# Kernel optimization log

Hardware: AMD Instinct MI355X
Metric: run time of the kernel (lower is better)

## Reference

```python
import jax, jax.numpy as jnp
import numpy as np

EPS = 1e-7


def ciou_pairwise(b1, b2):
    # b1: (N,1,4), b2: (1,N,4) in xyxy; returns (N,N) CIoU
    b1x1, b1y1, b1x2, b1y2 = b1[..., 0], b1[..., 1], b1[..., 2], b1[..., 3]
    b2x1, b2y1, b2x2, b2y2 = b2[..., 0], b2[..., 1], b2[..., 2], b2[..., 3]

    # intersection
    iw = jnp.clip(jnp.minimum(b1x2, b2x2) - jnp.maximum(b1x1, b2x1), 0.0)
    ih = jnp.clip(jnp.minimum(b1y2, b2y2) - jnp.maximum(b1y1, b2y1), 0.0)
    inter = iw * ih

    w1, h1 = b1x2 - b1x1, b1y2 - b1y1
    w2, h2 = b2x2 - b2x1, b2y2 - b2y1
    union = w1 * h1 + w2 * h2 - inter + EPS
    iou = inter / union

    # smallest enclosing box diagonal
    cw = jnp.maximum(b1x2, b2x2) - jnp.minimum(b1x1, b2x1)
    ch = jnp.maximum(b1y2, b2y2) - jnp.minimum(b1y1, b2y1)
    c2 = cw * cw + ch * ch + EPS

    # squared center distance
    rho2 = ((b2x1 + b2x2 - b1x1 - b1x2) ** 2 + (b2y1 + b2y2 - b1y1 - b1y2) ** 2) / 4.0

    # aspect-ratio consistency term
    v = (4.0 / (np.pi ** 2)) * (jnp.arctan(w2 / (h2 + EPS)) - jnp.arctan(w1 / (h1 + EPS))) ** 2
    alpha = jax.lax.stop_gradient(v / (v - iou + (1.0 + EPS)))
    return iou - (rho2 / c2 + v * alpha)


def setup_inputs() -> dict:
    key = jax.random.key(0)
    k1, k2, k3 = jax.random.split(key, 3)
    N = 4096
    conf = jax.random.uniform(k1, (N, 1), dtype=jnp.float32)           # confidence in [0,1)
    xy1 = jax.random.uniform(k2, (N, 2), dtype=jnp.float32) * 600.0    # top-left corner
    wh = jax.random.uniform(k3, (N, 2), dtype=jnp.float32) * 100.0 + 1.0  # width/height >= 1
    x = jnp.concatenate([conf, xy1, xy1 + wh], axis=1)                 # (N, 5): conf, x1, y1, x2, y2
    gamma = jnp.zeros((1,), dtype=jnp.float32)
    return {"x": x, "gamma": gamma}


def reference(x, gamma):
    boxes = x[:, 1:]
    conf = x[:, 0]
    iou = ciou_pairwise(boxes[:, None, :], boxes[None, :, :])          # (N, N)
    conf_matrix = conf[:, None] * conf[None, :]                        # (N, N) outer product
    attention = jax.nn.softmax(iou * conf_matrix, axis=-1)             # (N, N)
    x_prime = x * gamma + attention @ x                                # (N, 5)
    return jax.nn.sigmoid(x_prime)
```

## Files before the change

### kernel.cpp

```cpp
#include <hip/hip_runtime.h>
#include <math.h>

#define N 4096
#define FEPS 1e-7f
#define HEPS 5e-8f
#define BLK 256
#define JT 64
#define CH (N / JT)
#define N6 (N * 6)
#define KATAN 0.6366197723675814f
#define SQL2E 1.2011224087864498f


__global__ __launch_bounds__(BLK) void ciou_attn_kernel(
        const float* __restrict__ x,
        float* __restrict__ part) {
    __shared__ float4 jrec[CH * 3];
    const int tid = threadIdx.x;
    const int gb = blockIdx.x / JT;
    const int jt = blockIdx.x % JT;
    const int i = gb * BLK + tid;

    if (tid < CH) {
        int j = jt * CH + tid;
        float cf = x[j * 5 + 0], jx1 = x[j * 5 + 1], jy1 = x[j * 5 + 2];
        float jx2 = x[j * 5 + 3], jy2 = x[j * 5 + 4];
        float w = jx2 - jx1, h = jy2 - jy1;
        jrec[tid * 3 + 0] = make_float4(jx1, jy1, jx2, jy2);
        jrec[tid * 3 + 1] = make_float4((jx1 + jx2) * 0.5f, (jy1 + jy2) * 0.5f, w, h);
        jrec[tid * 3 + 2] = make_float4(fmaf(w, h, HEPS),
                                        KATAN * atanf(w / (h + FEPS)),
                                        cf * SQL2E, cf);
    }

    {
    }
    float cfr = x[i * 5 + 0];
    const float rx1 = x[i * 5 + 1], ry1 = x[i * 5 + 2];
    const float rx2 = x[i * 5 + 3], ry2 = x[i * 5 + 4];
    const float rw = rx2 - rx1, rh = ry2 - ry1;
    const float rhx = (rx1 + rx2) * 0.5f, rhy = (ry1 + ry2) * 0.5f;
    const float rareps = fmaf(rw, rh, HEPS);
    const float rat = KATAN * atanf(rw / (rh + FEPS));
    const float rcf2 = cfr * SQL2E;

    __syncthreads();

    float sum = 0.f, a0 = 0.f, a1 = 0.f, a2 = 0.f, a3 = 0.f, a4 = 0.f;
    const float ONEP = 1.f + FEPS;

    float4 A = jrec[0], B = jrec[1], C = jrec[2];
#pragma unroll 4
    for (int jj = 0; jj < CH; jj++) {
        const int nx = ((jj + 1) & (CH - 1)) * 3;
        float4 nA = jrec[nx + 0];
        float4 nB = jrec[nx + 1];
        float4 nC = jrec[nx + 2];

        float iwr = fminf(rx2, A.z) - fmaxf(rx1, A.x);
        float ihr = fminf(ry2, A.w) - fmaxf(ry1, A.y);
        float iw = fmaxf(iwr, 0.f);
        float ih = fmaxf(ihr, 0.f);
        float inter = iw * ih;
        float uni = (rareps + C.x) - inter;
        float cw = (rw + B.z) - iwr;
        float chh = (rh + B.w) - ihr;
        float c2 = fmaf(cw, cw, fmaf(chh, chh, FEPS));
        float dx = B.x - rhx;
        float dy = B.y - rhy;
        float rho2 = fmaf(dx, dx, dy * dy);
        float da = C.y - rat;
        float v = da * da;
        float P = fmaf(v + ONEP, uni, -inter);
        P = fmaxf(P, 1e-12f);
        float uc = uni * c2;
        float rr = __builtin_amdgcn_rcpf(uc * P);
        float t1 = fmaf(inter, c2, -(rho2 * uni));
        float vu = v * uni;
        float n2 = (vu * vu) * c2;
        float num = fmaf(t1, P, -n2);
        float s = (num * rr) * (rcf2 * C.z);
        float e = __builtin_amdgcn_exp2f(s);
        sum += e;
        a0 = fmaf(e, C.w, a0);
        a1 = fmaf(e, A.x, a1);
        a2 = fmaf(e, A.y, a2);
        a3 = fmaf(e, A.z, a3);
        a4 = fmaf(e, A.w, a4);

        A = nA; B = nB; C = nC;
    }

    float* p = part + (size_t)jt * N6 + (size_t)i * 6;
    p[0] = sum; p[1] = a0; p[2] = a1; p[3] = a2; p[4] = a3; p[5] = a4;
}

__global__ void epilogue_kernel(const float* __restrict__ x,
                                const float* __restrict__ gamma,
                                const float* __restrict__ part,
                                float* __restrict__ out) {
    int idx = blockIdx.x * blockDim.x + threadIdx.x;
    if (idx >= N * 5) return;
    int i = idx / 5, c = idx % 5;
    float se = 0.f, a = 0.f;
    const float* p = part + (size_t)i * 6;
#pragma unroll 8
    for (int jt = 0; jt < JT; jt++) {
        se += p[jt * (size_t)N6 + 0];
        a  += p[jt * (size_t)N6 + 1 + c];
    }
    float xp = x[idx] * gamma[0] + a / se;
    out[idx] = 1.f / (1.f + expf(-xp));
}

extern "C" void kernel_launch(void* const* d_in, const int* in_sizes, int n_in,
                              void* d_out, int out_size, void* d_ws, size_t ws_size,
                              hipStream_t stream) {
    const float* x = (const float*)d_in[0];
    const float* gamma = (const float*)d_in[1];
    float* out = (float*)d_out;
    float* part = (float*)d_ws;

    ciou_attn_kernel<<<(N / BLK) * JT, BLK, 0, stream>>>(x, part);
    epilogue_kernel<<<(N * 5 + 255) / 256, 256, 0, stream>>>(x, gamma, part, out);
}
```

Before: 83.70 us.

## Exploit pairwise symmetry with wave-level tile rotation via ds_bpermute

Computes each unordered box pair once by assigning waves to 64x64 tile pairs. Column boxes and column accumulators rotate across lanes with ds_bpermute, so both row and column softmax partials come from one exponent. This roughly halves the pairwise CIoU/exp work. In exchange it adds twelve cross-lane permutes per step, doubles the accumulation FMAs and the partial-sum workspace, and the epilogue now reduces over twice as many slots in a transposed, coalesced layout.

Result: slower. 95.06 us (+13.6%).

```diff
diff --git a/kernel.cpp b/kernel.cpp
--- a/kernel.cpp
+++ b/kernel.cpp
@@ -2,97 +2,119 @@
 #include <math.h>
 
 #define N 4096
+#define T 64
+#define NT (N / T)
+#define NSLOT (NT * 2)
 #define FEPS 1e-7f
 #define HEPS 5e-8f
 #define BLK 256
-#define JT 64
-#define CH (N / JT)
-#define N6 (N * 6)
 #define KATAN 0.6366197723675814f
 #define SQL2E 1.2011224087864498f
+#define ISQL2E 0.8325546111576977f
 
 
-__global__ __launch_bounds__(BLK) void ciou_attn_kernel(
+__device__ __forceinline__ float bperm(int addr, float v) {
+    return __int_as_float(__builtin_amdgcn_ds_bpermute(addr, __float_as_int(v)));
+}
+
+__global__ __launch_bounds__(BLK) void ciou_sym_kernel(
         const float* __restrict__ x,
         float* __restrict__ part) {
-    __shared__ float4 jrec[CH * 3];
-    const int tid = threadIdx.x;
-    const int gb = blockIdx.x / JT;
-    const int jt = blockIdx.x % JT;
-    const int i = gb * BLK + tid;
+    const int lane = threadIdx.x & 63;
+    const int w = blockIdx.x * (BLK / 64) + (threadIdx.x >> 6);
 
-    if (tid < CH) {
-        int j = jt * CH + tid;
-        float cf = x[j * 5 + 0], jx1 = x[j * 5 + 1], jy1 = x[j * 5 + 2];
-        float jx2 = x[j * 5 + 3], jy2 = x[j * 5 + 4];
-        float w = jx2 - jx1, h = jy2 - jy1;
-        jrec[tid * 3 + 0] = make_float4(jx1, jy1, jx2, jy2);
-        jrec[tid * 3 + 1] = make_float4((jx1 + jx2) * 0.5f, (jy1 + jy2) * 0.5f, w, h);
-        jrec[tid * 3 + 2] = make_float4(fmaf(w, h, HEPS),
-                                        KATAN * atanf(w / (h + FEPS)),
-                                        cf * SQL2E, cf);
+    int ta, tb, k0, iters, diag;
+    if (w < NT) {
+        ta = w; tb = w; k0 = 0; iters = T; diag = 1;
+    } else {
+        int m = w - NT;
+        int p = m >> 1, kh = m & 1;
+        int a = 0, rem = p;
+        while (rem >= NT - 1 - a) { rem -= NT - 1 - a; a++; }
+        ta = a; tb = a + 1 + rem; k0 = kh << 5; iters = 32; diag = 0;
     }
+    const int kh = k0 >> 5;
+    const int slot_row = diag ? (ta * 2)     : (tb * 2 + kh);
+    const int slot_col = diag ? (ta * 2 + 1) : (ta * 2 + kh);
 
-    {
-    }
-    float cfr = x[i * 5 + 0];
+    const int i = ta * T + lane;
+    const float rcf = x[i * 5 + 0];
     const float rx1 = x[i * 5 + 1], ry1 = x[i * 5 + 2];
     const float rx2 = x[i * 5 + 3], ry2 = x[i * 5 + 4];
     const float rw = rx2 - rx1, rh = ry2 - ry1;
     const float rhx = (rx1 + rx2) * 0.5f, rhy = (ry1 + ry2) * 0.5f;
     const float rareps = fmaf(rw, rh, HEPS);
     const float rat = KATAN * atanf(rw / (rh + FEPS));
-    const float rcf2 = cfr * SQL2E;
+    const float rcf2 = rcf * SQL2E;
 
-    __syncthreads();
+    const int j = tb * T + ((lane + k0) & 63);
+    float jx1 = x[j * 5 + 1], jy1 = x[j * 5 + 2];
+    float jx2 = x[j * 5 + 3], jy2 = x[j * 5 + 4];
+    float jat = KATAN * atanf((jx2 - jx1) / ((jy2 - jy1) + FEPS));
+    float jcf2 = x[j * 5 + 0] * SQL2E;
 
-    float sum = 0.f, a0 = 0.f, a1 = 0.f, a2 = 0.f, a3 = 0.f, a4 = 0.f;
+    const int nxt = ((lane + 1) & 63) * 4;
     const float ONEP = 1.f + FEPS;
 
-    float4 A = jrec[0], B = jrec[1], C = jrec[2];
-#pragma unroll 4
-    for (int jj = 0; jj < CH; jj++) {
-        const int nx = ((jj + 1) & (CH - 1)) * 3;
-        float4 nA = jrec[nx + 0];
-        float4 nB = jrec[nx + 1];
-        float4 nC = jrec[nx + 2];
+    float rs = 0.f, r0 = 0.f, r1 = 0.f, r2 = 0.f, r3 = 0.f, r4 = 0.f;
+    float cs = 0.f, c0 = 0.f, c1 = 0.f, c2a = 0.f, c3 = 0.f, c4 = 0.f;
 
-        float iwr = fminf(rx2, A.z) - fmaxf(rx1, A.x);
-        float ihr = fminf(ry2, A.w) - fmaxf(ry1, A.y);
-        float iw = fmaxf(iwr, 0.f);
-        float ih = fmaxf(ihr, 0.f);
-        float inter = iw * ih;
-        float uni = (rareps + C.x) - inter;
-        float cw = (rw + B.z) - iwr;
-        float chh = (rh + B.w) - ihr;
+#pragma unroll 2
+    for (int k = 0; k < iters; k++) {
+        float jw = jx2 - jx1, jh = jy2 - jy1;
+        float jareps = fmaf(jw, jh, HEPS);
+        float dx = fmaf(0.5f, jx1 + jx2, -rhx);
+        float dy = fmaf(0.5f, jy1 + jy2, -rhy);
+
+        float iwr = fminf(rx2, jx2) - fmaxf(rx1, jx1);
+        float ihr = fminf(ry2, jy2) - fmaxf(ry1, jy1);
+        float inter = fmaxf(iwr, 0.f) * fmaxf(ihr, 0.f);
+        float uni = (rareps + jareps) - inter;
+        float cw = (rw + jw) - iwr;
+        float chh = (rh + jh) - ihr;
         float c2 = fmaf(cw, cw, fmaf(chh, chh, FEPS));
-        float dx = B.x - rhx;
-        float dy = B.y - rhy;
         float rho2 = fmaf(dx, dx, dy * dy);
-        float da = C.y - rat;
+        float da = jat - rat;
         float v = da * da;
         float P = fmaf(v + ONEP, uni, -inter);
         P = fmaxf(P, 1e-12f);
-        float uc = uni * c2;
-        float rr = __builtin_amdgcn_rcpf(uc * P);
+        float rr = __builtin_amdgcn_rcpf(uni * c2 * P);
         float t1 = fmaf(inter, c2, -(rho2 * uni));
         float vu = v * uni;
-        float n2 = (vu * vu) * c2;
-        float num = fmaf(t1, P, -n2);
-        float s = (num * rr) * (rcf2 * C.z);
-        float e = __builtin_amdgcn_exp2f(s);
-        sum += e;
-        a0 = fmaf(e, C.w, a0);
-        a1 = fmaf(e, A.x, a1);
-        a2 = fmaf(e, A.y, a2);
-        a3 = fmaf(e, A.z, a3);
-        a4 = fmaf(e, A.w, a4);
+        float num = fmaf(t1, P, -((vu * vu) * c2));
+        float e = __builtin_amdgcn_exp2f((num * rr) * (rcf2 * jcf2));
 
-        A = nA; B = nB; C = nC;
+        rs += e;
+        r0 = fmaf(e, jcf2, r0);
+        r1 = fmaf(e, jx1, r1);
+        r2 = fmaf(e, jy1, r2);
+        r3 = fmaf(e, jx2, r3);
+        r4 = fmaf(e, jy2, r4);
+
+        cs += e;
+        c0 = fmaf(e, rcf, c0);
+        c1 = fmaf(e, rx1, c1);
+        c2a = fmaf(e, ry1, c2a);
+        c3 = fmaf(e, rx2, c3);
+        c4 = fmaf(e, ry2, c4);
+
+        jx1 = bperm(nxt, jx1); jy1 = bperm(nxt, jy1);
+        jx2 = bperm(nxt, jx2); jy2 = bperm(nxt, jy2);
+        jat = bperm(nxt, jat); jcf2 = bperm(nxt, jcf2);
+        cs = bperm(nxt, cs);   c0 = bperm(nxt, c0);  c1 = bperm(nxt, c1);
+        c2a = bperm(nxt, c2a); c3 = bperm(nxt, c3);  c4 = bperm(nxt, c4);
     }
 
-    float* p = part + (size_t)jt * N6 + (size_t)i * 6;
-    p[0] = sum; p[1] = a0; p[2] = a1; p[3] = a2; p[4] = a3; p[5] = a4;
+    r0 *= ISQL2E;
+    float* pr = part + (size_t)slot_row * 6 * N;
+    pr[0 * N + i] = rs; pr[1 * N + i] = r0; pr[2 * N + i] = r1;
+    pr[3 * N + i] = r2; pr[4 * N + i] = r3; pr[5 * N + i] = r4;
+
+    const int jr = tb * T + ((lane + k0 + iters) & 63);
+    float* pc = part + (size_t)slot_col * 6 * N;
+    if (diag) { cs = c0 = c1 = c2a = c3 = c4 = 0.f; }
+    pc[0 * N + jr] = cs; pc[1 * N + jr] = c0; pc[2 * N + jr] = c1;
+    pc[3 * N + jr] = c2a; pc[4 * N + jr] = c3; pc[5 * N + jr] = c4;
 }
 
 __global__ void epilogue_kernel(const float* __restrict__ x,
@@ -103,11 +125,10 @@
     if (idx >= N * 5) return;
     int i = idx / 5, c = idx % 5;
     float se = 0.f, a = 0.f;
-    const float* p = part + (size_t)i * 6;
 #pragma unroll 8
-    for (int jt = 0; jt < JT; jt++) {
-        se += p[jt * (size_t)N6 + 0];
-        a  += p[jt * (size_t)N6 + 1 + c];
+    for (int s = 0; s < NSLOT; s++) {
+        se += part[((size_t)s * 6 + 0) * N + i];
+        a  += part[((size_t)s * 6 + 1 + c) * N + i];
     }
     float xp = x[idx] * gamma[0] + a / se;
     out[idx] = 1.f / (1.f + expf(-xp));
@@ -121,6 +142,6 @@
     float* out = (float*)d_out;
     float* part = (float*)d_ws;
 
-    ciou_attn_kernel<<<(N / BLK) * JT, BLK, 0, stream>>>(x, part);
+    ciou_sym_kernel<<<(NT + 2 * (NT * (NT - 1) / 2)) / (BLK / 64), BLK, 0, stream>>>(x, part);
     epilogue_kernel<<<(N * 5 + 255) / 256, 256, 0, stream>>>(x, gamma, part, out);
 }
```
